# Kernel tuning notes

Measured on AMD Instinct MI355X. Metric: run time of the kernel, lower is better.

The kernel has to match this reference:

```python
import jax, jax.numpy as jnp
import numpy as np
from jax import lax

N, T, I, H, O = 2048, 512, 32, 64, 1

def setup_inputs() -> dict:
    key = jax.random.key(0)
    ks = jax.random.split(key, 7)
    s_ih = 1.0 / np.sqrt(H)
    return {
        "x": jax.random.normal(ks[0], (N, T, I), dtype=jnp.float32),
        "W_ih": jax.random.uniform(ks[1], (H, I), jnp.float32, -s_ih, s_ih),
        "W_hh": jax.random.uniform(ks[2], (H, H), jnp.float32, -s_ih, s_ih),
        "b_ih": jax.random.uniform(ks[3], (H,), jnp.float32, -s_ih, s_ih),
        "b_hh": jax.random.uniform(ks[4], (H,), jnp.float32, -s_ih, s_ih),
        "fc_w": jax.random.uniform(ks[5], (O, H), jnp.float32, -s_ih, s_ih),
        "fc_b": jax.random.uniform(ks[6], (O,), jnp.float32, -s_ih, s_ih),
    }

def reference(x, W_ih, W_hh, b_ih, b_hh, fc_w, fc_b):
    # Batched equivalent of the per-sample python loop: each sample starts
    # from the same hidden state of ones (self.hidden = torch.ones(...)).
    n, t = x.shape[0], x.shape[1]
    h0 = jnp.ones((n, W_hh.shape[0]), dtype=x.dtype)
    xs = jnp.swapaxes(x, 0, 1)  # [T, N, I] -> scan over time

    def step(h, xt):
        # Elman RNN with tanh (torch nn.RNN default nonlinearity)
        h_new = jnp.tanh(xt @ W_ih.T + b_ih + h @ W_hh.T + b_hh)
        return h_new, None

    hT, _ = lax.scan(step, h0, xs)  # hT: [N, H], last-timestep hidden = out[-1]
    return jax.nn.sigmoid(hT @ fc_w.T + fc_b)  # [N, O]
```

## Files before the change

kernel.cpp:

```cpp
#include <hip/hip_runtime.h>


#define RN 2048
#define RT 512
#define RI 32
#define RH 64

typedef _Float16 h4 __attribute__((ext_vector_type(4)));
typedef float    f4 __attribute__((ext_vector_type(4)));

__device__ __forceinline__ void lds_barrier() {
    asm volatile("s_waitcnt lgkmcnt(0)\n\ts_barrier" ::: "memory");
}

__device__ __forceinline__ int pk2(float a, float b) {
    return __builtin_bit_cast(int, __builtin_amdgcn_cvt_pkrtz(a, b));
}
__device__ __forceinline__ h4 pack4(float a, float b, float c, float d) {
    union { h4 v; int i[2]; } u;
    u.i[0] = pk2(a, b);
    u.i[1] = pk2(c, d);
    return u.v;
}
__device__ __forceinline__ h4 packf4(f4 v) { return pack4(v[0], v[1], v[2], v[3]); }

__device__ __forceinline__ float tanh_fast(float z) {
    float e = __expf(2.0f * z);
    return 1.0f - __fdividef(2.0f, e + 1.0f);
}

__global__ __launch_bounds__(256, 1) void rnn_mfma4(
    const float* __restrict__ x,
    const float* __restrict__ W_ih,
    const float* __restrict__ W_hh,
    const float* __restrict__ b_ih,
    const float* __restrict__ b_hh,
    const float* __restrict__ fc_w,
    const float* __restrict__ fc_b,
    float* __restrict__ out)
{
    const int tid  = threadIdx.x;
    const int w    = tid >> 6;
    const int lane = tid & 63;
    const int col  = lane & 15;
    const int quad = lane >> 4;
    const int g    = blockIdx.x;

    __shared__ unsigned long long hb[2][4 * 64];
    __shared__ float ob[4][16];

    h4 Ahh[4];
#pragma unroll
    for (int kt = 0; kt < 4; ++kt) {
        f4 v = *(const f4*)(W_hh + (w * 16 + col) * RH + kt * 16 + quad * 4);
        Ahh[kt] = packf4(v);
    }
    h4 Aih[2];
#pragma unroll
    for (int kt = 0; kt < 2; ++kt) {
        f4 v = *(const f4*)(W_ih + (w * 16 + col) * RI + kt * 16 + quad * 4);
        Aih[kt] = packf4(v);
    }
    f4 biasv;
    {
        f4 bi = *(const f4*)(b_ih + w * 16 + quad * 4);
        f4 bh = *(const f4*)(b_hh + w * 16 + quad * 4);
        biasv = bi + bh;
    }

    const float* xb = x + (size_t)(g * 16 + col) * (RT * RI);
    f4 xbuf[4][2];
#pragma unroll
    for (int s = 0; s < 4; ++s) {
        xbuf[s][0] = *(const f4*)(xb + s * RI + quad * 4);
        xbuf[s][1] = *(const f4*)(xb + s * RI + 16 + quad * 4);
    }

    h4 Bh[4];
#pragma unroll
    for (int kt = 0; kt < 4; ++kt) Bh[kt] = pack4(1.f, 1.f, 1.f, 1.f);
    f4 hv;

    for (int t4 = 0; t4 < RT; t4 += 4) {
#pragma unroll
        for (int s = 0; s < 4; ++s) {
            const int t = t4 + s;
            h4 bx0 = packf4(xbuf[s][0]);
            h4 bx1 = packf4(xbuf[s][1]);
            int tn = t + 4; if (tn > RT - 1) tn = RT - 1;
            xbuf[s][0] = *(const f4*)(xb + tn * RI + quad * 4);
            xbuf[s][1] = *(const f4*)(xb + tn * RI + 16 + quad * 4);

            f4 c0 = __builtin_amdgcn_mfma_f32_16x16x16f16(Aih[0], bx0, biasv, 0, 0, 0);
            f4 c1 = __builtin_amdgcn_mfma_f32_16x16x16f16(Aih[1], bx1, f4{0.f, 0.f, 0.f, 0.f}, 0, 0, 0);
            c0 = __builtin_amdgcn_mfma_f32_16x16x16f16(Ahh[0], Bh[0], c0, 0, 0, 0);
            c1 = __builtin_amdgcn_mfma_f32_16x16x16f16(Ahh[1], Bh[1], c1, 0, 0, 0);
            c0 = __builtin_amdgcn_mfma_f32_16x16x16f16(Ahh[2], Bh[2], c0, 0, 0, 0);
            c1 = __builtin_amdgcn_mfma_f32_16x16x16f16(Ahh[3], Bh[3], c1, 0, 0, 0);
            f4 acc = c0 + c1;

            hv[0] = tanh_fast(acc[0]);
            hv[1] = tanh_fast(acc[1]);
            hv[2] = tanh_fast(acc[2]);
            hv[3] = tanh_fast(acc[3]);

            const int p = t & 1;
            hb[p][w * 64 + lane] = __builtin_bit_cast(unsigned long long, packf4(hv));
            lds_barrier();
            Bh[0] = __builtin_bit_cast(h4, hb[p][0 * 64 + lane]);
            Bh[1] = __builtin_bit_cast(h4, hb[p][1 * 64 + lane]);
            Bh[2] = __builtin_bit_cast(h4, hb[p][2 * 64 + lane]);
            Bh[3] = __builtin_bit_cast(h4, hb[p][3 * 64 + lane]);
        }
    }

    {
        f4 wv = *(const f4*)(fc_w + w * 16 + quad * 4);
        float s = wv[0] * hv[0] + wv[1] * hv[1] + wv[2] * hv[2] + wv[3] * hv[3];
        s += __shfl_xor(s, 16, 64);
        s += __shfl_xor(s, 32, 64);
        if (quad == 0) ob[w][col] = s;
        lds_barrier();
        if (w == 0 && lane < 16) {
            float logit = ob[0][lane] + ob[1][lane] + ob[2][lane] + ob[3][lane] + fc_b[0];
            out[g * 16 + lane] = __fdividef(1.0f, 1.0f + __expf(-logit));
        }
    }
}

extern "C" void kernel_launch(void* const* d_in, const int* in_sizes, int n_in,
                              void* d_out, int out_size, void* d_ws, size_t ws_size,
                              hipStream_t stream) {
    rnn_mfma4<<<RN / 16, 256, 0, stream>>>(
        (const float*)d_in[0], (const float*)d_in[1], (const float*)d_in[2],
        (const float*)d_in[3], (const float*)d_in[4], (const float*)d_in[5],
        (const float*)d_in[6], (float*)d_out);
}
```

Baseline: 311.1 us.

## Precompute next step's input projection before the barrier, off the recurrence path

The input projection W_ih·x_{t+1} + bias is now computed one step ahead, placed after the hidden-state LDS store and before the barrier. Each timestep's critical chain then holds only the four W_hh MFMAs, the tanh and the LDS exchange. The x prefetch ring is re-indexed to load t+5, and tanh is rewritten with exp2, rcp and fma intrinsics to shorten the dependent math. In exchange, register pressure rises slightly and there is one extra MFMA chain per step running in the shadow of the barrier.

```diff
diff --git a/kernel.cpp b/kernel.cpp
--- a/kernel.cpp
+++ b/kernel.cpp
@@ -25,11 +25,12 @@
 __device__ __forceinline__ h4 packf4(f4 v) { return pack4(v[0], v[1], v[2], v[3]); }
 
 __device__ __forceinline__ float tanh_fast(float z) {
-    float e = __expf(2.0f * z);
-    return 1.0f - __fdividef(2.0f, e + 1.0f);
+    float e = __builtin_amdgcn_exp2f(z * 2.88539008177792681472f);
+    float r = __builtin_amdgcn_rcpf(e + 1.0f);
+    return __builtin_fmaf(-2.0f, r, 1.0f);
 }
 
-__global__ __launch_bounds__(256, 1) void rnn_mfma4(
+__global__ __launch_bounds__(256, 1) void rnn_mfma7(
     const float* __restrict__ x,
     const float* __restrict__ W_ih,
     const float* __restrict__ W_hh,
@@ -71,9 +72,19 @@
     const float* xb = x + (size_t)(g * 16 + col) * (RT * RI);
     f4 xbuf[4][2];
 #pragma unroll
-    for (int s = 0; s < 4; ++s) {
+    for (int s = 1; s < 4; ++s) {
         xbuf[s][0] = *(const f4*)(xb + s * RI + quad * 4);
         xbuf[s][1] = *(const f4*)(xb + s * RI + 16 + quad * 4);
+    }
+    xbuf[0][0] = *(const f4*)(xb + 4 * RI + quad * 4);
+    xbuf[0][1] = *(const f4*)(xb + 4 * RI + 16 + quad * 4);
+
+    f4 cx;
+    {
+        f4 x0a = *(const f4*)(xb + quad * 4);
+        f4 x0b = *(const f4*)(xb + 16 + quad * 4);
+        cx = __builtin_amdgcn_mfma_f32_16x16x16f16(Aih[0], packf4(x0a), biasv, 0, 0, 0);
+        cx = __builtin_amdgcn_mfma_f32_16x16x16f16(Aih[1], packf4(x0b), cx, 0, 0, 0);
     }
 
     h4 Bh[4];
@@ -85,16 +96,9 @@
 #pragma unroll
         for (int s = 0; s < 4; ++s) {
             const int t = t4 + s;
-            h4 bx0 = packf4(xbuf[s][0]);
-            h4 bx1 = packf4(xbuf[s][1]);
-            int tn = t + 4; if (tn > RT - 1) tn = RT - 1;
-            xbuf[s][0] = *(const f4*)(xb + tn * RI + quad * 4);
-            xbuf[s][1] = *(const f4*)(xb + tn * RI + 16 + quad * 4);
 
-            f4 c0 = __builtin_amdgcn_mfma_f32_16x16x16f16(Aih[0], bx0, biasv, 0, 0, 0);
-            f4 c1 = __builtin_amdgcn_mfma_f32_16x16x16f16(Aih[1], bx1, f4{0.f, 0.f, 0.f, 0.f}, 0, 0, 0);
-            c0 = __builtin_amdgcn_mfma_f32_16x16x16f16(Ahh[0], Bh[0], c0, 0, 0, 0);
-            c1 = __builtin_amdgcn_mfma_f32_16x16x16f16(Ahh[1], Bh[1], c1, 0, 0, 0);
+            f4 c0 = __builtin_amdgcn_mfma_f32_16x16x16f16(Ahh[0], Bh[0], cx, 0, 0, 0);
+            f4 c1 = __builtin_amdgcn_mfma_f32_16x16x16f16(Ahh[1], Bh[1], f4{0.f, 0.f, 0.f, 0.f}, 0, 0, 0);
             c0 = __builtin_amdgcn_mfma_f32_16x16x16f16(Ahh[2], Bh[2], c0, 0, 0, 0);
             c1 = __builtin_amdgcn_mfma_f32_16x16x16f16(Ahh[3], Bh[3], c1, 0, 0, 0);
             f4 acc = c0 + c1;
@@ -106,11 +110,22 @@
 
             const int p = t & 1;
             hb[p][w * 64 + lane] = __builtin_bit_cast(unsigned long long, packf4(hv));
+
+            const int sn = (s + 1) & 3;
+            h4 bx0 = packf4(xbuf[sn][0]);
+            h4 bx1 = packf4(xbuf[sn][1]);
+            int tl = t + 5; if (tl > RT - 1) tl = RT - 1;
+            xbuf[sn][0] = *(const f4*)(xb + tl * RI + quad * 4);
+            xbuf[sn][1] = *(const f4*)(xb + tl * RI + 16 + quad * 4);
+            f4 cxn = __builtin_amdgcn_mfma_f32_16x16x16f16(Aih[0], bx0, biasv, 0, 0, 0);
+            cxn = __builtin_amdgcn_mfma_f32_16x16x16f16(Aih[1], bx1, cxn, 0, 0, 0);
+
             lds_barrier();
             Bh[0] = __builtin_bit_cast(h4, hb[p][0 * 64 + lane]);
             Bh[1] = __builtin_bit_cast(h4, hb[p][1 * 64 + lane]);
             Bh[2] = __builtin_bit_cast(h4, hb[p][2 * 64 + lane]);
             Bh[3] = __builtin_bit_cast(h4, hb[p][3 * 64 + lane]);
+            cx = cxn;
         }
     }
 
@@ -131,7 +146,7 @@
 extern "C" void kernel_launch(void* const* d_in, const int* in_sizes, int n_in,
                               void* d_out, int out_size, void* d_ws, size_t ws_size,
                               hipStream_t stream) {
-    rnn_mfma4<<<RN / 16, 256, 0, stream>>>(
+    rnn_mfma7<<<RN / 16, 256, 0, stream>>>(
         (const float*)d_in[0], (const float*)d_in[1], (const float*)d_in[2],
         (const float*)d_in[3], (const float*)d_in[4], (const float*)d_in[5],
         (const float*)d_in[6], (float*)d_out);
```

New measurement: 335.3 us. +7.8%, slower.
